# Kernel tuning notes

Measured on AMD Instinct MI355X. Metric: run time of the kernel, lower is better.

## Reference

```python
import jax, jax.numpy as jnp
import numpy as np

LN_EPS = 1e-5


def setup_inputs() -> dict:
    key = jax.random.key(0)
    ks = jax.random.split(key, 10)
    B, T, D, K = 32, 1024, 512, 3
    enc = jax.random.normal(ks[0], (B, T, D), jnp.float32)
    dur = jax.random.randint(ks[1], (B, T), 0, 7, jnp.int32)
    s = 0.02
    return {
        "encoder_output": enc,
        "duration_target": dur,
        "conv1_w": jax.random.normal(ks[2], (K, D, D), jnp.float32) * s,  # HIO layout
        "conv1_b": jnp.zeros((D,), jnp.float32),
        "ln1_w": jnp.ones((D,), jnp.float32),
        "ln1_b": jnp.zeros((D,), jnp.float32),
        "conv2_w": jax.random.normal(ks[3], (K, D, D), jnp.float32) * s,
        "conv2_b": jnp.zeros((D,), jnp.float32),
        "ln2_w": jnp.ones((D,), jnp.float32),
        "ln2_b": jnp.zeros((D,), jnp.float32),
        "lin_w": jax.random.normal(ks[4], (D, 1), jnp.float32) * s,
        "lin_b": jnp.zeros((1,), jnp.float32),
        "max_len": 4096,
    }


def _conv_relu(x, w, b):
    # x: [B,T,D], w: [K, D_in, D_out] ('HIO'), 'SAME' padding == torch padding=1 for k=3
    y = jax.lax.conv_general_dilated(
        x, w, window_strides=(1,), padding="SAME",
        dimension_numbers=("NHC", "HIO", "NHC"))
    return jax.nn.relu(y + b)


def _layernorm(x, g, b):
    mu = jnp.mean(x, axis=-1, keepdims=True)
    var = jnp.mean(jnp.square(x - mu), axis=-1, keepdims=True)
    return (x - mu) * jax.lax.rsqrt(var + LN_EPS) * g + b


def reference(encoder_output, duration_target, conv1_w, conv1_b, ln1_w, ln1_b,
              conv2_w, conv2_b, ln2_w, ln2_b, lin_w, lin_b, max_len):
    B, T, D = encoder_output.shape
    # duration predictor: conv -> relu -> LN -> conv -> relu -> LN -> linear
    h = _layernorm(_conv_relu(encoder_output, conv1_w, conv1_b), ln1_w, ln1_b)
    h = _layernorm(_conv_relu(h, conv2_w, conv2_b), ln2_w, ln2_b)
    duration_predictor_output = (h @ lin_w + lin_b)[..., 0]  # [B,T]

    # training path: expand by duration_target via fused gather with cumulative offsets
    cum = jnp.cumsum(duration_target, axis=1)          # [B,T]
    pos = jnp.arange(max_len, dtype=jnp.int32)         # [L]
    # src index for output frame j: first t with cum[t] > j
    idx = jax.vmap(lambda c: jnp.searchsorted(c, pos, side="right"))(cum)  # [B,L]
    valid = pos[None, :] < cum[:, -1:]                  # [B,L]
    idx = jnp.minimum(idx, T - 1)
    expanded = jnp.take_along_axis(encoder_output, idx[:, :, None], axis=1)
    expanded = expanded * valid[:, :, None].astype(encoder_output.dtype)
    return expanded, duration_predictor_output
```

## Files before the change

### kernel.cpp

```cpp
#include <hip/hip_runtime.h>
#include <hip/hip_bf16.h>

#define BB 32
#define TT 1024
#define DD 512
#define LL 4096
#define KDIM 1536
#define TP 1026
#define ROWS (BB * TT)
#define NT (KDIM / 32)

typedef __attribute__((ext_vector_type(8))) short short8;
typedef __attribute__((ext_vector_type(8))) unsigned short ushort8;
typedef __attribute__((ext_vector_type(4))) float floatx4;

__device__ __forceinline__ unsigned short f2bf(float f) {
  unsigned int u = __builtin_bit_cast(unsigned int, f);
  u += 0x7FFF + ((u >> 16) & 1);
  return (unsigned short)(u >> 16);
}
__device__ __forceinline__ float bf2f(unsigned short h) {
  return __builtin_bit_cast(float, (unsigned int)h << 16);
}

#define GLOAD_LDS16(g, l)                                          \
  __builtin_amdgcn_global_load_lds(                                \
      (const __attribute__((address_space(1))) void*)(g),          \
      (__attribute__((address_space(3))) void*)(l), 16, 0, 0)

#define PAD_BLKS ((BB * TP) / 4)
#define W0 (PAD_BLKS + 16)
#define C0 (W0 + 384)
#define PREP_BLKS (C0 + 32)

__global__ __launch_bounds__(256) void prep_kernel(
    const float* __restrict__ X, unsigned short* __restrict__ Xp,
    unsigned short* __restrict__ Hp,
    const float* __restrict__ W1, unsigned short* __restrict__ Wt1,
    const float* __restrict__ W2, unsigned short* __restrict__ Wt2,
    const int* __restrict__ dur, int* __restrict__ cum) {
  __shared__ float tile[64][65];
  const int tid = threadIdx.x;
  const int lane = tid & 63;

  if (blockIdx.x >= C0) {
    int* ls = reinterpret_cast<int*>(tile);
    const int b = blockIdx.x - C0;
    int4 v = reinterpret_cast<const int4*>(dur + b * TT)[tid];
    const int s0 = v.x, s1 = s0 + v.y, s2 = s1 + v.z, s3 = s2 + v.w;
    ls[tid] = s3;
    __syncthreads();
    for (int off = 1; off < 256; off <<= 1) {
      int x = (tid >= off) ? ls[tid - off] : 0;
      __syncthreads();
      ls[tid] += x;
      __syncthreads();
    }
    const int base = tid ? ls[tid - 1] : 0;
    int4 o = {base + s0, base + s1, base + s2, base + s3};
    reinterpret_cast<int4*>(cum + b * TT)[tid] = o;
    return;
  }
  if (blockIdx.x >= W0) {
    const int w = blockIdx.x - W0;
    const int z = w / 192;
    const int rem = w - z * 192;
    const int bx = rem & 7;
    const int by = rem >> 3;
    const float* W = z ? W2 : W1;
    unsigned short* Wt = z ? Wt2 : Wt1;
    const int n0 = bx * 64;
    const int k0 = by * 64;
    const int c = lane;
    const int r4 = tid >> 6;
#pragma unroll
    for (int r = 0; r < 16; ++r)
      tile[r * 4 + r4][c] = W[(long)(k0 + r * 4 + r4) * DD + n0 + c];
    __syncthreads();
#pragma unroll
    for (int r = 0; r < 16; ++r)
      Wt[(long)(n0 + r * 4 + r4) * KDIM + k0 + c] = f2bf(tile[c][r * 4 + r4]);
    return;
  }
  if (blockIdx.x >= PAD_BLKS) {
    const int hid = (blockIdx.x - PAD_BLKS) * 4 + (tid >> 6);
    const int b = hid >> 1;
    const long r = (long)b * TP + ((hid & 1) ? (TP - 1) : 0);
    *reinterpret_cast<ushort8*>(Hp + r * DD + lane * 8) = (ushort8)0;
    return;
  }
  const int row = blockIdx.x * 4 + (tid >> 6);
  const int b  = row / TP;
  const int pr = row - b * TP;
  ushort8* o = reinterpret_cast<ushort8*>(Xp + (long)row * DD + lane * 8);
  ushort8 v;
  if (pr == 0 || pr == TP - 1) {
    v = (ushort8)0;
  } else {
    const float* p = X + ((long)(b * TT + pr - 1)) * DD + lane * 8;
    float4 a = *reinterpret_cast<const float4*>(p);
    float4 c = *reinterpret_cast<const float4*>(p + 4);
    v[0] = f2bf(a.x); v[1] = f2bf(a.y); v[2] = f2bf(a.z); v[3] = f2bf(a.w);
    v[4] = f2bf(c.x); v[5] = f2bf(c.y); v[6] = f2bf(c.z); v[7] = f2bf(c.w);
  }
  *o = v;
}

template <int LAYER>
__global__ __launch_bounds__(512, 2) void fused_conv_ln_kernel(
    const unsigned short* __restrict__ Xp, const unsigned short* __restrict__ Wt,
    const float* __restrict__ bias, const float* __restrict__ g,
    const float* __restrict__ be, const float* __restrict__ lw,
    const float* __restrict__ lb, unsigned short* __restrict__ Hp,
    float* __restrict__ dpo) {
  __shared__ unsigned short As[3][128 * 32];
  __shared__ unsigned short Bs[3][512 * 32];
  __shared__ float sS[4][128];
  __shared__ float sQ[4][128];
  __shared__ float muL[128];
  __shared__ float rsL[128];

  const int tid  = threadIdx.x;
  const int lane = tid & 63;
  const int wid  = tid >> 6;
  const int srow = lane >> 2;
  const int gchunk = (lane & 3) ^ (srow & 3);
  const int frow = lane & 15;
  const int quad = lane >> 4;
  const int rdch = quad ^ (frow & 3);
  const int wm = (wid >> 2) * 64;
  const int wn = (wid & 3) * 128;
  const int wc = wid & 3;

  const int m0 = blockIdx.x * 128;
  const int bA = m0 >> 10;
  const int t0 = m0 & (TT - 1);

  const unsigned short* gA0 =
      Xp + (long)(bA * TP + t0 + wid * 16 + srow) * DD + gchunk * 8;
  const unsigned short* gB0 =
      Wt + (long)(wid * 16 + srow) * KDIM + gchunk * 8;

  floatx4 acc[4][8];
#pragma unroll
  for (int i = 0; i < 4; ++i)
#pragma unroll
    for (int j = 0; j < 8; ++j) acc[i][j] = (floatx4){0.f, 0.f, 0.f, 0.f};

#define STAGE(bi, kk)                                                         \
  do {                                                                        \
    const int tap_ = (kk) >> 9;                                               \
    const int c0_  = (kk) & 511;                                              \
    GLOAD_LDS16(gA0 + (long)tap_ * DD + c0_, &As[bi][(wid * 16) * 32]);       \
    GLOAD_LDS16(gB0 + (kk),                   &Bs[bi][(wid * 16) * 32]);      \
    GLOAD_LDS16(gB0 + (long)128 * KDIM + (kk), &Bs[bi][(128 + wid * 16) * 32]); \
    GLOAD_LDS16(gB0 + (long)256 * KDIM + (kk), &Bs[bi][(256 + wid * 16) * 32]); \
    GLOAD_LDS16(gB0 + (long)384 * KDIM + (kk), &Bs[bi][(384 + wid * 16) * 32]); \
  } while (0)

#define COMPUTE(bi)                                                           \
  do {                                                                        \
    short8 a_[4], b_[8];                                                      \
    _Pragma("unroll")                                                         \
    for (int i = 0; i < 4; ++i)                                               \
      a_[i] = *reinterpret_cast<const short8*>(                               \
          &As[bi][(wm + i * 16 + frow) * 32 + rdch * 8]);                     \
    _Pragma("unroll")                                                         \
    for (int j = 0; j < 8; ++j)                                               \
      b_[j] = *reinterpret_cast<const short8*>(                               \
          &Bs[bi][(wn + j * 16 + frow) * 32 + rdch * 8]);                     \
    _Pragma("unroll")                                                         \
    for (int i = 0; i < 4; ++i)                                               \
      _Pragma("unroll")                                                       \
      for (int j = 0; j < 8; ++j)                                             \
        acc[i][j] = __builtin_amdgcn_mfma_f32_16x16x32_bf16(                  \
            a_[i], b_[j], acc[i][j], 0, 0, 0);                                \
  } while (0)

  STAGE(0, 0);
  STAGE(1, 32);

  int cur = 0;
  int stg = 2;
  for (int t = 0; t < NT - 1; ++t) {
    asm volatile("s_waitcnt vmcnt(5)" ::: "memory");
    __builtin_amdgcn_s_barrier();
    __builtin_amdgcn_sched_barrier(0);
    if (t + 2 < NT) STAGE(stg, (t + 2) * 32);
    COMPUTE(cur);
    cur = (cur == 2) ? 0 : cur + 1;
    stg = (stg == 2) ? 0 : stg + 1;
  }
  asm volatile("s_waitcnt vmcnt(0)" ::: "memory");
  __builtin_amdgcn_s_barrier();
  __builtin_amdgcn_sched_barrier(0);
  COMPUTE(cur);
#undef STAGE
#undef COMPUTE

  float bz[8];
#pragma unroll
  for (int j = 0; j < 8; ++j) bz[j] = bias[wn + j * 16 + frow];
#pragma unroll
  for (int i = 0; i < 4; ++i)
#pragma unroll
    for (int j = 0; j < 8; ++j)
#pragma unroll
      for (int r = 0; r < 4; ++r)
        acc[i][j][r] = fmaxf(acc[i][j][r] + bz[j], 0.f);

  float ps[16], pq[16];
#pragma unroll
  for (int i = 0; i < 4; ++i)
#pragma unroll
    for (int r = 0; r < 4; ++r) {
      float s = 0.f, q = 0.f;
#pragma unroll
      for (int j = 0; j < 8; ++j) {
        const float v = acc[i][j][r];
        s += v; q += v * v;
      }
      ps[i * 4 + r] = s; pq[i * 4 + r] = q;
    }
#pragma unroll
  for (int off = 1; off < 16; off <<= 1)
#pragma unroll
    for (int k = 0; k < 16; ++k) {
      ps[k] += __shfl_xor(ps[k], off);
      pq[k] += __shfl_xor(pq[k], off);
    }
  if (frow == 0) {
#pragma unroll
    for (int i = 0; i < 4; ++i)
#pragma unroll
      for (int r = 0; r < 4; ++r) {
        const int row = wm + i * 16 + quad * 4 + r;
        sS[wc][row] = ps[i * 4 + r];
        sQ[wc][row] = pq[i * 4 + r];
      }
  }
  __syncthreads();
  if (tid < 128) {
    const float s = sS[0][tid] + sS[1][tid] + sS[2][tid] + sS[3][tid];
    const float q = sQ[0][tid] + sQ[1][tid] + sQ[2][tid] + sQ[3][tid];
    const float mu = s * (1.f / DD);
    const float var = q * (1.f / DD) - mu * mu;
    muL[tid] = mu;
    rsL[tid] = rsqrtf(var + 1e-5f);
  }
  __syncthreads();

  float gg[8], bb[8];
#pragma unroll
  for (int j = 0; j < 8; ++j) {
    gg[j] = g[wn + j * 16 + frow];
    bb[j] = be[wn + j * 16 + frow];
  }

  if constexpr (LAYER == 1) {
    unsigned short* Ls = &Bs[0][0];
    const int h = wm >> 6;
#pragma unroll
    for (int ph = 0; ph < 2; ++ph) {
      __syncthreads();
      if (h == ph) {
#pragma unroll
        for (int i = 0; i < 4; ++i)
#pragma unroll
          for (int r = 0; r < 4; ++r) {
            const int row = wm + i * 16 + quad * 4 + r;
            const float mu = muL[row];
            const float rs = rsL[row];
            const int lrow = row - ph * 64;
#pragma unroll
            for (int j = 0; j < 8; ++j) {
              const float v = (acc[i][j][r] - mu) * rs * gg[j] + bb[j];
              Ls[lrow * 520 + wn + j * 16 + frow] = f2bf(v);
            }
          }
      }
      __syncthreads();
      const long gbase = (long)(bA * TP + t0 + ph * 64 + 1) * DD;
#pragma unroll
      for (int it = 0; it < 8; ++it) {
        const int r2 = it * 8 + wid;
        const int cc = lane * 8;
        ushort8 val = *reinterpret_cast<const ushort8*>(&Ls[r2 * 520 + cc]);
        *reinterpret_cast<ushort8*>(&Hp[gbase + (long)r2 * DD + cc]) = val;
      }
    }
  } else {
    float ww[8];
#pragma unroll
    for (int j = 0; j < 8; ++j) ww[j] = lw[wn + j * 16 + frow];
#pragma unroll
    for (int i = 0; i < 4; ++i)
#pragma unroll
      for (int r = 0; r < 4; ++r) {
        const int row = wm + i * 16 + quad * 4 + r;
        const float mu = muL[row];
        const float rs = rsL[row];
        float d = 0.f;
#pragma unroll
        for (int j = 0; j < 8; ++j) {
          const float v = (acc[i][j][r] - mu) * rs * gg[j] + bb[j];
          d += v * ww[j];
        }
#pragma unroll
        for (int off = 1; off < 16; off <<= 1) d += __shfl_xor(d, off);
        if (frow == 0) sS[wc][row] = d;
      }
    __syncthreads();
    if (tid < 128)
      dpo[m0 + tid] =
          sS[0][tid] + sS[1][tid] + sS[2][tid] + sS[3][tid] + lb[0];
  }
}

__global__ __launch_bounds__(512) void gather_kernel(
    const float* __restrict__ X, const int* __restrict__ cum,
    float* __restrict__ out) {
  const long gf = (long)blockIdx.x * 4 + (threadIdx.x >> 7);
  const int tl = threadIdx.x & 127;
  const int b = (int)(gf >> 12);
  const int j = (int)(gf & (LL - 1));
  const int* c = cum + b * TT;
  floatx4* o = reinterpret_cast<floatx4*>(out + gf * DD) + tl;
  const int total = c[TT - 1];
  if (j >= total) {
    __builtin_nontemporal_store((floatx4){0.f, 0.f, 0.f, 0.f}, o);
    return;
  }
  int lo = 0, hi = TT - 1;
  while (lo < hi) {
    const int mid = (lo + hi) >> 1;
    if (c[mid] <= j) lo = mid + 1; else hi = mid;
  }
  const floatx4* src =
      reinterpret_cast<const floatx4*>(X + ((long)b * TT + lo) * DD) + tl;
  __builtin_nontemporal_store(*src, o);
}

extern "C" void kernel_launch(void* const* d_in, const int* in_sizes, int n_in,
                              void* d_out, int out_size, void* d_ws,
                              size_t ws_size, hipStream_t stream) {
  const float* enc = (const float*)d_in[0];
  const int* dur   = (const int*)d_in[1];
  const float* w1  = (const float*)d_in[2];
  const float* b1  = (const float*)d_in[3];
  const float* g1  = (const float*)d_in[4];
  const float* be1 = (const float*)d_in[5];
  const float* w2  = (const float*)d_in[6];
  const float* b2  = (const float*)d_in[7];
  const float* g2  = (const float*)d_in[8];
  const float* be2 = (const float*)d_in[9];
  const float* lw  = (const float*)d_in[10];
  const float* lb  = (const float*)d_in[11];

  float* out = (float*)d_out;
  float* expanded = out;
  float* dpo = out + (long)BB * LL * DD;

  unsigned short* enc_pad = (unsigned short*)(expanded);
  unsigned short* h1_pad  = (unsigned short*)(expanded + 9000000);
  unsigned short* wt1     = (unsigned short*)(expanded + 18000000);
  unsigned short* wt2     = (unsigned short*)(expanded + 18400000);
  int* cum = (int*)d_ws;

  prep_kernel<<<PREP_BLKS, 256, 0, stream>>>(enc, enc_pad, h1_pad, w1, wt1,
                                             w2, wt2, dur, cum);

  fused_conv_ln_kernel<1><<<ROWS / 128, 512, 0, stream>>>(
      enc_pad, wt1, b1, g1, be1, nullptr, nullptr, h1_pad, nullptr);
  fused_conv_ln_kernel<2><<<ROWS / 128, 512, 0, stream>>>(
      h1_pad, wt2, b2, g2, be2, lw, lb, nullptr, dpo);

  gather_kernel<<<BB * LL / 4, 512, 0, stream>>>(enc, cum, expanded);
}
```

Measured before the change: 542.4 us.

## Fuse prep, two conv-LN layers and gather into one cooperative persistent kernel

Replaces four separate launches with one cooperative kernel of 256 blocks that runs padding/weight transposition/scan, both conv+LayerNorm phases, and the expansion gather, separated by grid syncs. The duration scan now also materialises a per-frame source index table so the gather avoids a binary search per output frame. This aims to remove launch gaps and search overhead, but adds grid-wide barriers, fixes the grid size for the memory-bound gather, and drops nontemporal stores for the large output.

```diff
diff --git a/kernel.cpp b/kernel.cpp
--- a/kernel.cpp
+++ b/kernel.cpp
@@ -1,5 +1,8 @@
 #include <hip/hip_runtime.h>
 #include <hip/hip_bf16.h>
+#include <hip/hip_cooperative_groups.h>
+
+namespace cg = cooperative_groups;
 
 #define BB 32
 #define TT 1024
@@ -19,108 +22,39 @@
   u += 0x7FFF + ((u >> 16) & 1);
   return (unsigned short)(u >> 16);
 }
-__device__ __forceinline__ float bf2f(unsigned short h) {
-  return __builtin_bit_cast(float, (unsigned int)h << 16);
-}
 
 #define GLOAD_LDS16(g, l)                                          \
   __builtin_amdgcn_global_load_lds(                                \
       (const __attribute__((address_space(1))) void*)(g),          \
       (__attribute__((address_space(3))) void*)(l), 16, 0, 0)
 
-#define PAD_BLKS ((BB * TP) / 4)
-#define W0 (PAD_BLKS + 16)
-#define C0 (W0 + 384)
-#define PREP_BLKS (C0 + 32)
-
-__global__ __launch_bounds__(256) void prep_kernel(
-    const float* __restrict__ X, unsigned short* __restrict__ Xp,
-    unsigned short* __restrict__ Hp,
-    const float* __restrict__ W1, unsigned short* __restrict__ Wt1,
-    const float* __restrict__ W2, unsigned short* __restrict__ Wt2,
-    const int* __restrict__ dur, int* __restrict__ cum) {
-  __shared__ float tile[64][65];
-  const int tid = threadIdx.x;
-  const int lane = tid & 63;
-
-  if (blockIdx.x >= C0) {
-    int* ls = reinterpret_cast<int*>(tile);
-    const int b = blockIdx.x - C0;
-    int4 v = reinterpret_cast<const int4*>(dur + b * TT)[tid];
-    const int s0 = v.x, s1 = s0 + v.y, s2 = s1 + v.z, s3 = s2 + v.w;
-    ls[tid] = s3;
-    __syncthreads();
-    for (int off = 1; off < 256; off <<= 1) {
-      int x = (tid >= off) ? ls[tid - off] : 0;
-      __syncthreads();
-      ls[tid] += x;
-      __syncthreads();
-    }
-    const int base = tid ? ls[tid - 1] : 0;
-    int4 o = {base + s0, base + s1, base + s2, base + s3};
-    reinterpret_cast<int4*>(cum + b * TT)[tid] = o;
-    return;
-  }
-  if (blockIdx.x >= W0) {
-    const int w = blockIdx.x - W0;
-    const int z = w / 192;
-    const int rem = w - z * 192;
-    const int bx = rem & 7;
-    const int by = rem >> 3;
-    const float* W = z ? W2 : W1;
-    unsigned short* Wt = z ? Wt2 : Wt1;
-    const int n0 = bx * 64;
-    const int k0 = by * 64;
-    const int c = lane;
-    const int r4 = tid >> 6;
-#pragma unroll
-    for (int r = 0; r < 16; ++r)
-      tile[r * 4 + r4][c] = W[(long)(k0 + r * 4 + r4) * DD + n0 + c];
-    __syncthreads();
-#pragma unroll
-    for (int r = 0; r < 16; ++r)
-      Wt[(long)(n0 + r * 4 + r4) * KDIM + k0 + c] = f2bf(tile[c][r * 4 + r4]);
-    return;
-  }
-  if (blockIdx.x >= PAD_BLKS) {
-    const int hid = (blockIdx.x - PAD_BLKS) * 4 + (tid >> 6);
-    const int b = hid >> 1;
-    const long r = (long)b * TP + ((hid & 1) ? (TP - 1) : 0);
-    *reinterpret_cast<ushort8*>(Hp + r * DD + lane * 8) = (ushort8)0;
-    return;
-  }
-  const int row = blockIdx.x * 4 + (tid >> 6);
-  const int b  = row / TP;
-  const int pr = row - b * TP;
-  ushort8* o = reinterpret_cast<ushort8*>(Xp + (long)row * DD + lane * 8);
-  ushort8 v;
-  if (pr == 0 || pr == TP - 1) {
-    v = (ushort8)0;
-  } else {
-    const float* p = X + ((long)(b * TT + pr - 1)) * DD + lane * 8;
-    float4 a = *reinterpret_cast<const float4*>(p);
-    float4 c = *reinterpret_cast<const float4*>(p + 4);
-    v[0] = f2bf(a.x); v[1] = f2bf(a.y); v[2] = f2bf(a.z); v[3] = f2bf(a.w);
-    v[4] = f2bf(c.x); v[5] = f2bf(c.y); v[6] = f2bf(c.z); v[7] = f2bf(c.w);
-  }
-  *o = v;
-}
+struct MegaArgs {
+  const float* enc;
+  const int* dur;
+  const float* w1; const float* b1; const float* g1; const float* be1;
+  const float* w2; const float* b2; const float* g2; const float* be2;
+  const float* lw; const float* lb;
+  unsigned short* enc_pad;
+  unsigned short* h1_pad;
+  unsigned short* wt1;
+  unsigned short* wt2;
+  float* expanded;
+  float* dpo;
+  int* cum;
+  int* idx;
+};
 
 template <int LAYER>
-__global__ __launch_bounds__(512, 2) void fused_conv_ln_kernel(
+__device__ __forceinline__ void conv_ln_phase(
+    const int bid, const int tid,
     const unsigned short* __restrict__ Xp, const unsigned short* __restrict__ Wt,
     const float* __restrict__ bias, const float* __restrict__ g,
     const float* __restrict__ be, const float* __restrict__ lw,
     const float* __restrict__ lb, unsigned short* __restrict__ Hp,
-    float* __restrict__ dpo) {
-  __shared__ unsigned short As[3][128 * 32];
-  __shared__ unsigned short Bs[3][512 * 32];
-  __shared__ float sS[4][128];
-  __shared__ float sQ[4][128];
-  __shared__ float muL[128];
-  __shared__ float rsL[128];
-
-  const int tid  = threadIdx.x;
+    float* __restrict__ dpo,
+    unsigned short (&As)[3][128 * 32], unsigned short (&Bs)[3][512 * 32],
+    float (&sS)[4][128], float (&sQ)[4][128],
+    float (&muL)[128], float (&rsL)[128]) {
   const int lane = tid & 63;
   const int wid  = tid >> 6;
   const int srow = lane >> 2;
@@ -132,7 +66,7 @@
   const int wn = (wid & 3) * 128;
   const int wc = wid & 3;
 
-  const int m0 = blockIdx.x * 128;
+  const int m0 = bid * 128;
   const int bA = m0 >> 10;
   const int t0 = m0 & (TT - 1);
 
@@ -312,68 +246,161 @@
       }
     __syncthreads();
     if (tid < 128)
-      dpo[m0 + tid] =
+      dpo[bid * 128 + tid] =
           sS[0][tid] + sS[1][tid] + sS[2][tid] + sS[3][tid] + lb[0];
   }
 }
 
-__global__ __launch_bounds__(512) void gather_kernel(
-    const float* __restrict__ X, const int* __restrict__ cum,
-    float* __restrict__ out) {
-  const long gf = (long)blockIdx.x * 4 + (threadIdx.x >> 7);
-  const int tl = threadIdx.x & 127;
-  const int b = (int)(gf >> 12);
-  const int j = (int)(gf & (LL - 1));
-  const int* c = cum + b * TT;
-  floatx4* o = reinterpret_cast<floatx4*>(out + gf * DD) + tl;
-  const int total = c[TT - 1];
-  if (j >= total) {
-    __builtin_nontemporal_store((floatx4){0.f, 0.f, 0.f, 0.f}, o);
-    return;
-  }
-  int lo = 0, hi = TT - 1;
-  while (lo < hi) {
-    const int mid = (lo + hi) >> 1;
-    if (c[mid] <= j) lo = mid + 1; else hi = mid;
-  }
-  const floatx4* src =
-      reinterpret_cast<const floatx4*>(X + ((long)b * TT + lo) * DD) + tl;
-  __builtin_nontemporal_store(*src, o);
+__global__ __launch_bounds__(512, 2) void mega_kernel(MegaArgs a) {
+  __shared__ unsigned short As[3][128 * 32];
+  __shared__ unsigned short Bs[3][512 * 32];
+  __shared__ float sS[4][128];
+  __shared__ float sQ[4][128];
+  __shared__ float muL[128];
+  __shared__ float rsL[128];
+
+  const int bid = blockIdx.x;
+  const int tid = threadIdx.x;
+  cg::grid_group grid = cg::this_grid();
+
+  {
+    const long NCH = (long)BB * TP * 64;
+    for (long c = bid * 512 + tid; c < NCH; c += 256 * 512) {
+      const int row = (int)(c >> 6);
+      const int col = ((int)c & 63) * 8;
+      const int b  = row / TP;
+      const int pr = row - b * TP;
+      ushort8 v;
+      if (pr == 0 || pr == TP - 1) {
+        v = (ushort8)0;
+        *reinterpret_cast<ushort8*>(a.h1_pad + (long)row * DD + col) = v;
+      } else {
+        const float* p = a.enc + ((long)(b * TT + pr - 1)) * DD + col;
+        float4 x0 = *reinterpret_cast<const float4*>(p);
+        float4 x1 = *reinterpret_cast<const float4*>(p + 4);
+        v[0] = f2bf(x0.x); v[1] = f2bf(x0.y); v[2] = f2bf(x0.z); v[3] = f2bf(x0.w);
+        v[4] = f2bf(x1.x); v[5] = f2bf(x1.y); v[6] = f2bf(x1.z); v[7] = f2bf(x1.w);
+      }
+      *reinterpret_cast<ushort8*>(a.enc_pad + (long)row * DD + col) = v;
+    }
+  }
+
+  {
+    float* wtf = reinterpret_cast<float*>(&Bs[0][0]);
+    const int cc = tid & 63;
+    const int r8 = tid >> 6;
+    for (int w = bid; w < 384; w += 256) {
+      const int z = (w >= 192);
+      const int rem = w - z * 192;
+      const int bx = rem & 7;
+      const int by = rem >> 3;
+      const float* W = z ? a.w2 : a.w1;
+      unsigned short* Wt = z ? a.wt2 : a.wt1;
+      const int n0 = bx * 64;
+      const int k0 = by * 64;
+      __syncthreads();
+#pragma unroll
+      for (int r = 0; r < 8; ++r)
+        wtf[(r * 8 + r8) * 65 + cc] = W[(long)(k0 + r * 8 + r8) * DD + n0 + cc];
+      __syncthreads();
+#pragma unroll
+      for (int r = 0; r < 8; ++r)
+        Wt[(long)(n0 + r * 8 + r8) * KDIM + k0 + cc] =
+            f2bf(wtf[cc * 65 + r * 8 + r8]);
+    }
+  }
+
+  if (bid < 32) {
+    int* scan = reinterpret_cast<int*>(&As[0][0]);
+    int2 v = reinterpret_cast<const int2*>(a.dur + bid * TT)[tid];
+    const int s0 = v.x, s1 = v.x + v.y;
+    scan[tid] = s1;
+    __syncthreads();
+    for (int off = 1; off < 512; off <<= 1) {
+      int x = (tid >= off) ? scan[tid - off] : 0;
+      __syncthreads();
+      scan[tid] += x;
+      __syncthreads();
+    }
+    const int base = tid ? scan[tid - 1] : 0;
+    reinterpret_cast<int2*>(a.cum + bid * TT)[tid] =
+        make_int2(base + s0, base + s1);
+    int* ib = a.idx + bid * LL;
+    const int e0 = min(base + v.x, LL);
+    for (int j = base; j < e0; ++j) ib[j] = 2 * tid;
+    const int e1 = min(base + s1, LL);
+    for (int j = base + v.x; j < e1; ++j) ib[j] = 2 * tid + 1;
+  }
+
+  __threadfence();
+  grid.sync();
+
+  conv_ln_phase<1>(bid, tid, a.enc_pad, a.wt1, a.b1, a.g1, a.be1,
+                   nullptr, nullptr, a.h1_pad, nullptr,
+                   As, Bs, sS, sQ, muL, rsL);
+
+  __threadfence();
+  grid.sync();
+
+  conv_ln_phase<2>(bid, tid, a.h1_pad, a.wt2, a.b2, a.g2, a.be2,
+                   a.lw, a.lb, nullptr, a.dpo,
+                   As, Bs, sS, sQ, muL, rsL);
+
+  __threadfence();
+  grid.sync();
+
+  {
+    const int tl = tid & 127;
+    const int sub = tid >> 7;
+    for (int fi = bid; fi < ROWS; fi += 256) {
+      const long gf = (long)fi * 4 + sub;
+      const int b = (int)(gf >> 12);
+      const int j = (int)(gf & (LL - 1));
+      const int total = a.cum[b * TT + TT - 1];
+      floatx4* o = reinterpret_cast<floatx4*>(a.expanded + gf * DD) + tl;
+      if (j >= total) {
+        *o = (floatx4){0.f, 0.f, 0.f, 0.f};
+      } else {
+        const int lo = a.idx[b * LL + j];
+        const floatx4* src =
+            reinterpret_cast<const floatx4*>(a.enc + ((long)b * TT + lo) * DD) +
+            tl;
+        *o = *src;
+      }
+    }
+  }
 }
 
 extern "C" void kernel_launch(void* const* d_in, const int* in_sizes, int n_in,
                               void* d_out, int out_size, void* d_ws,
                               size_t ws_size, hipStream_t stream) {
-  const float* enc = (const float*)d_in[0];
-  const int* dur   = (const int*)d_in[1];
-  const float* w1  = (const float*)d_in[2];
-  const float* b1  = (const float*)d_in[3];
-  const float* g1  = (const float*)d_in[4];
-  const float* be1 = (const float*)d_in[5];
-  const float* w2  = (const float*)d_in[6];
-  const float* b2  = (const float*)d_in[7];
-  const float* g2  = (const float*)d_in[8];
-  const float* be2 = (const float*)d_in[9];
-  const float* lw  = (const float*)d_in[10];
-  const float* lb  = (const float*)d_in[11];
-
   float* out = (float*)d_out;
   float* expanded = out;
   float* dpo = out + (long)BB * LL * DD;
 
-  unsigned short* enc_pad = (unsigned short*)(expanded);
-  unsigned short* h1_pad  = (unsigned short*)(expanded + 9000000);
-  unsigned short* wt1     = (unsigned short*)(expanded + 18000000);
-  unsigned short* wt2     = (unsigned short*)(expanded + 18400000);
-  int* cum = (int*)d_ws;
-
-  prep_kernel<<<PREP_BLKS, 256, 0, stream>>>(enc, enc_pad, h1_pad, w1, wt1,
-                                             w2, wt2, dur, cum);
-
-  fused_conv_ln_kernel<1><<<ROWS / 128, 512, 0, stream>>>(
-      enc_pad, wt1, b1, g1, be1, nullptr, nullptr, h1_pad, nullptr);
-  fused_conv_ln_kernel<2><<<ROWS / 128, 512, 0, stream>>>(
-      h1_pad, wt2, b2, g2, be2, lw, lb, nullptr, dpo);
-
-  gather_kernel<<<BB * LL / 4, 512, 0, stream>>>(enc, cum, expanded);
+  MegaArgs a;
+  a.enc = (const float*)d_in[0];
+  a.dur = (const int*)d_in[1];
+  a.w1  = (const float*)d_in[2];
+  a.b1  = (const float*)d_in[3];
+  a.g1  = (const float*)d_in[4];
+  a.be1 = (const float*)d_in[5];
+  a.w2  = (const float*)d_in[6];
+  a.b2  = (const float*)d_in[7];
+  a.g2  = (const float*)d_in[8];
+  a.be2 = (const float*)d_in[9];
+  a.lw  = (const float*)d_in[10];
+  a.lb  = (const float*)d_in[11];
+  a.enc_pad = (unsigned short*)(expanded);
+  a.h1_pad  = (unsigned short*)(expanded + 9000000);
+  a.wt1     = (unsigned short*)(expanded + 18000000);
+  a.wt2     = (unsigned short*)(expanded + 18400000);
+  a.expanded = expanded;
+  a.dpo = dpo;
+  a.cum = (int*)d_ws;
+  a.idx = (int*)d_ws + ROWS;
+
+  void* params[] = {&a};
+  hipLaunchCooperativeKernel((const void*)mega_kernel, dim3(256), dim3(512),
+                             params, 0, stream);
 }
```

Result: slower. 808.9 us (+49.1%).
